# Kernel optimization log

Measured on AMD Instinct MI355X. Metric: run time of the kernel, lower is better.

## Reference

```python
import jax, jax.numpy as jnp
import numpy as np

# Config matching init_kwargs: N=4 networks, dims 128 -> 1024 -> 1024 -> 512
A, B, D = 8, 2048, 128     # agents, batch, input size
N = 4                       # number of independent SePS networks
H1, H2, H3 = 1024, 1024, 512


def setup_inputs() -> dict:
    key = jax.random.key(0)
    ks = jax.random.split(key, 6)
    inputs = jax.random.normal(ks[0], (A, B, D), dtype=jnp.float32)  # stacked per-agent obs
    seps_indices = jax.random.randint(ks[1], (B, A), 0, N)           # cluster id per (sample, agent)
    scale = lambda k, shape, fan: jax.random.normal(k, shape, dtype=jnp.float32) * (1.0 / np.sqrt(fan))
    W0 = scale(ks[2], (N, D, H1), D);   b0 = jnp.zeros((N, H1), jnp.float32)
    W1 = scale(ks[3], (N, H1, H2), H1); b1 = jnp.zeros((N, H2), jnp.float32)
    W2 = scale(ks[4], (N, H2, H3), H2); b2 = jnp.zeros((N, H3), jnp.float32)
    return {"inputs": inputs, "seps_indices": seps_indices,
            "W0": W0, "b0": b0, "W1": W1, "b1": b1, "W2": W2, "b2": b2}


def reference(inputs, seps_indices, W0, b0, W1, b1, W2, b2):
    # Run every network densely on the full stacked input, as the torch module does.
    # inputs: [A, B, D]; W*: [N, in, out]
    h = jax.nn.relu(jnp.einsum('abd,ndh->nabh', inputs, W0) + b0[:, None, None, :])
    h = jax.nn.relu(jnp.einsum('nabh,nhk->nabk', h, W1) + b1[:, None, None, :])
    out_all = jnp.einsum('nabk,nko->nabo', h, W2) + b2[:, None, None, :]  # [N, A, B, H3]
    # Gather along the network axis per (agent, sample): seps_indices is [B, A]
    idx = seps_indices.T                              # [A, B]
    a = jnp.arange(inputs.shape[0])[:, None]          # [A, 1]
    b = jnp.arange(inputs.shape[1])[None, :]          # [1, B]
    return out_all[idx, a, b, :]                      # [A, B, H3] (stacked per-agent outputs)
```

## Files before the change

### kernel.cpp

```cpp
#include <hip/hip_runtime.h>
#include <hip/hip_bf16.h>

#define AG 8
#define BT 2048
#define RT (AG*BT)
#define NNET 4
#define D0 128
#define H1 1024
#define H2 1024
#define H3 512

#define XBLK 40

typedef __attribute__((ext_vector_type(8))) short short8;
typedef __attribute__((ext_vector_type(4))) float f32x4;

__device__ __forceinline__ unsigned short f2bf(float f){
  unsigned int x = __float_as_uint(f);
  x += 0x7fff + ((x >> 16) & 1);
  return (unsigned short)(x >> 16);
}

template<int N> __device__ __forceinline__ void vmw(){
  if constexpr (N==8)      asm volatile("s_waitcnt vmcnt(8)" ::: "memory");
  else if constexpr (N==4) asm volatile("s_waitcnt vmcnt(4)" ::: "memory");
  else                     asm volatile("s_waitcnt vmcnt(0)" ::: "memory");
}

__device__ __forceinline__ void gload_lds16(const void* g, void* l){
  __builtin_amdgcn_global_load_lds(
      (const __attribute__((address_space(1))) unsigned int*)g,
      (__attribute__((address_space(3))) unsigned int*)l, 16, 0, 0);
}

__device__ __forceinline__ int bucket_off(const int* counts, int n){
  int s = 0;
  #pragma unroll
  for (int i = 0; i < NNET-1; i++) if (i < n) s += counts[i];
  return s;
}

__global__ void k_init(int* counts){
  if (threadIdx.x < NNET) counts[threadIdx.x] = 0;
}

__global__ __launch_bounds__(256) void k_compact(const int* __restrict__ seps,
                          int* __restrict__ counts, int* __restrict__ rowlist){
  __shared__ int lcount[NNET];
  __shared__ int lbase[NNET];
  int t = blockIdx.x * 256 + threadIdx.x;
  if (threadIdx.x < NNET) lcount[threadIdx.x] = 0;
  __syncthreads();
  int a = t >> 11, b = t & (BT-1);
  int n = seps[b*AG + a];
  int lrank = atomicAdd(&lcount[n], 1);
  __syncthreads();
  if (threadIdx.x < NNET)
    lbase[threadIdx.x] = atomicAdd(&counts[threadIdx.x], lcount[threadIdx.x]);
  __syncthreads();
  rowlist[n*RT + lbase[n] + lrank] = t;
}

template<int K, int NOUT>
__global__ __launch_bounds__(256) void k_transpose(const float* __restrict__ W,
                                                   unsigned short* __restrict__ WT){
  __shared__ float tile[32][33];
  int n = blockIdx.z;
  int k0 = blockIdx.x*32, o0 = blockIdx.y*32;
  const float* Wn = W + (size_t)n*K*NOUT;
  unsigned short* WTn = WT + (size_t)n*NOUT*K;
  int tx = threadIdx.x & 31, ty0 = threadIdx.x >> 5;
  #pragma unroll
  for (int r = 0; r < 32; r += 8)
    tile[ty0 + r][tx] = Wn[(size_t)(k0 + ty0 + r)*NOUT + o0 + tx];
  __syncthreads();
  #pragma unroll
  for (int r = 0; r < 32; r += 8)
    WTn[(size_t)(o0 + ty0 + r)*K + k0 + tx] = f2bf(tile[tx][ty0 + r]);
}

__global__ __launch_bounds__(256) void k_gather0(const float* __restrict__ X,
                          const int* __restrict__ counts,
                          const int* __restrict__ rowlist, unsigned short* __restrict__ X0h){
  int n = blockIdx.y;
  int cnt = counts[n];
  int i = blockIdx.x*16 + (threadIdx.x >> 4);
  if (i >= cnt) return;
  int off = bucket_off(counts, n);
  int orig = rowlist[n*RT + i];
  int c = (threadIdx.x & 15) * 8;
  const float* src = X + (size_t)orig*D0 + c;
  float4 v0 = *(const float4*)src, v1 = *(const float4*)(src+4);
  ushort4 u0, u1;
  u0.x=f2bf(v0.x); u0.y=f2bf(v0.y); u0.z=f2bf(v0.z); u0.w=f2bf(v0.w);
  u1.x=f2bf(v1.x); u1.y=f2bf(v1.y); u1.z=f2bf(v1.z); u1.w=f2bf(v1.w);
  unsigned short* dst = X0h + (size_t)(off + i)*D0 + c;
  *(ushort4*)dst = u0; *(ushort4*)(dst+4) = u1;
}

template<int K, int NOUT, int RELU, int SCATTER>
__global__ __launch_bounds__(256, 3) void k_mlp(
    const unsigned short* __restrict__ X,
    const unsigned short* __restrict__ WT,
    const float* __restrict__ Bias,
    const int* __restrict__ counts,
    const int* __restrict__ rowlist,
    unsigned short* __restrict__ Yh,
    float* __restrict__ Yf)
{
  constexpr int T = K / 32;
  const int n = blockIdx.z;
  const int cnt = counts[n];
  const int i0 = blockIdx.x * 128;
  if (i0 >= cnt) return;
  const int off = bucket_off(counts, n);
  const int bn = blockIdx.y * 128;

  __shared__ __align__(16) unsigned short As[3][128*32];
  __shared__ __align__(16) unsigned short Bs[3][128*32];
  __shared__ int rs[128];

  const int t = threadIdx.x, lane = t & 63, wave = t >> 6;
  const int wm = wave >> 1, wn = wave & 1;
  const int lr = lane & 15, g = lane >> 4;

  if (SCATTER && t < 128) rs[t] = rowlist[n*RT + min(i0 + t, cnt-1)];

  const unsigned short* pA[2]; const unsigned short* pB[2];
  unsigned int ldsoff[2];
  const unsigned short* WTn = WT + (size_t)n * NOUT * K;
  #pragma unroll
  for (int j = 0; j < 2; j++){
    int r  = (j*4 + wave)*16 + (lane >> 2);
    int ps = lane & 3;
    int ls = ps ^ ((r >> 1) & 3);
    int rA = min(i0 + r, cnt-1);
    pA[j] = X   + (size_t)(off + rA)*K + ls*8;
    pB[j] = WTn + (size_t)(bn  + r )*K + ls*8;
    ldsoff[j] = (unsigned)(j*4 + wave) * 512;
  }

  int aoff[4], boff[4];
  #pragma unroll
  for (int i = 0; i < 4; i++){
    int ra = wm*64 + i*16 + lr;
    aoff[i] = ra*32 + (g ^ ((ra>>1)&3))*8;
    int rb = wn*64 + i*16 + lr;
    boff[i] = rb*32 + (g ^ ((rb>>1)&3))*8;
  }

  __syncthreads();

  #pragma unroll
  for (int s = 0; s < 3; ++s){
    #pragma unroll
    for (int j = 0; j < 2; j++){
      gload_lds16(pA[j], &As[s][ldsoff[j]]);
      gload_lds16(pB[j], &Bs[s][ldsoff[j]]);
      pA[j] += 32; pB[j] += 32;
    }
  }

  f32x4 acc[4][4] = {};
  int b = 0;
  for (int ks = 0; ks < T; ++ks){
    if (ks < T-2)       vmw<8>();
    else if (ks == T-2) vmw<4>();
    else                vmw<0>();
    __builtin_amdgcn_s_barrier();

    short8 av[4], bv[4];
    #pragma unroll
    for (int i = 0; i < 4; i++) av[i] = *(const short8*)&As[b][aoff[i]];
    #pragma unroll
    for (int i = 0; i < 4; i++) bv[i] = *(const short8*)&Bs[b][boff[i]];

    #pragma unroll
    for (int mi = 0; mi < 4; mi++)
      #pragma unroll
      for (int ni = 0; ni < 4; ni++)
        acc[mi][ni] = __builtin_amdgcn_mfma_f32_16x16x32_bf16(bv[ni], av[mi], acc[mi][ni], 0, 0, 0);
    asm volatile("s_waitcnt lgkmcnt(0)" ::: "memory");
    __builtin_amdgcn_s_barrier();
    if (ks + 3 < T){
      #pragma unroll
      for (int j = 0; j < 2; j++){
        gload_lds16(pA[j], &As[b][ldsoff[j]]);
        gload_lds16(pB[j], &Bs[b][ldsoff[j]]);
        pA[j] += 32; pB[j] += 32;
      }
    }

    b = (b == 2) ? 0 : b + 1;
  }

  f32x4 bias4[4];
  #pragma unroll
  for (int ni = 0; ni < 4; ni++)
    bias4[ni] = *(const f32x4*)&Bias[n*NOUT + bn + wn*64 + ni*16 + (g<<2)];

  #pragma unroll
  for (int mi = 0; mi < 4; mi++){
    int rloc = wm*64 + mi*16 + lr;
    int grow = i0 + rloc;
    if (grow < cnt){
      #pragma unroll
      for (int ni = 0; ni < 4; ni++){
        float o[4];
        #pragma unroll
        for (int i = 0; i < 4; i++){
          float v = acc[mi][ni][i] + bias4[ni][i];
          if (RELU) v = fmaxf(v, 0.f);
          o[i] = v;
        }
        int cb = bn + wn*64 + ni*16 + (g<<2);
        if (SCATTER){
          *(float4*)&Yf[(size_t)rs[rloc]*NOUT + cb] = make_float4(o[0],o[1],o[2],o[3]);
        } else {
          ushort4 u;
          u.x=f2bf(o[0]); u.y=f2bf(o[1]); u.z=f2bf(o[2]); u.w=f2bf(o[3]);
          *(ushort4*)&Yh[(size_t)(off + grow)*NOUT + cb] = u;
        }
      }
    }
  }
}

extern "C" void kernel_launch(void* const* d_in, const int* in_sizes, int n_in,
                              void* d_out, int out_size, void* d_ws, size_t ws_size,
                              hipStream_t stream) {
  const float* inputs = (const float*)d_in[0];
  const int*   seps   = (const int*)  d_in[1];
  const float* W0     = (const float*)d_in[2];
  const float* b0     = (const float*)d_in[3];
  const float* W1     = (const float*)d_in[4];
  const float* b1     = (const float*)d_in[5];
  const float* W2     = (const float*)d_in[6];
  const float* b2     = (const float*)d_in[7];
  float* out = (float*)d_out;

  char* ws = (char*)d_ws;
  int* counts  = (int*)ws;
  int* rowlist = (int*)(ws + 4096);
  const size_t MB = 1u << 20;
  unsigned short* WT0 = (unsigned short*)(ws + 1*MB);
  unsigned short* WT1 = (unsigned short*)(ws + 2*MB);
  unsigned short* WT2 = (unsigned short*)(ws + 10*MB);
  unsigned short* h1  = (unsigned short*)(ws + 14*MB);
  unsigned short* h2  = (unsigned short*)(ws + 46*MB);
  unsigned short* X0h = (unsigned short*)(ws + 46*MB);

  k_init   <<<1, 64, 0, stream>>>(counts);
  k_compact<<<RT/256, 256, 0, stream>>>(seps, counts, rowlist);

  k_transpose<D0, H1><<<dim3(D0/32, H1/32, NNET), 256, 0, stream>>>(W0, WT0);
  k_transpose<H1, H2><<<dim3(H1/32, H2/32, NNET), 256, 0, stream>>>(W1, WT1);
  k_transpose<H2, H3><<<dim3(H2/32, H3/32, NNET), 256, 0, stream>>>(W2, WT2);
  k_gather0<<<dim3(RT/16, NNET), 256, 0, stream>>>(inputs, counts, rowlist, X0h);

  k_mlp<D0, H1, 1, 0><<<dim3(XBLK, H1/128, NNET), 256, 0, stream>>>(
      X0h, WT0, b0, counts, rowlist, h1, nullptr);
  k_mlp<H1, H2, 1, 0><<<dim3(XBLK, H2/128, NNET), 256, 0, stream>>>(
      h1, WT1, b1, counts, rowlist, h2, nullptr);
  k_mlp<H2, H3, 0, 1><<<dim3(XBLK, H3/128, NNET), 256, 0, stream>>>(
      h2, WT2, b2, counts, rowlist, nullptr, out);
}
```

Before: 135.5 us.

## Replace LDS-staged triple-buffered GEMM loads with direct global register loads

Removes the shared-memory tiles, the async global-to-LDS pipeline and the per-step barriers from the MLP GEMM kernel. Each wave now loads its A and B MFMA fragments straight from global memory into registers and relies on the cache for reuse across waves. This drops LDS traffic and synchronisation, but each tile is fetched from global memory or cache several times and there is no explicit prefetch to hide latency. The occupancy hint in the launch bounds is also removed.

```diff
diff --git a/kernel.cpp b/kernel.cpp
--- a/kernel.cpp
+++ b/kernel.cpp
@@ -19,18 +19,6 @@
   unsigned int x = __float_as_uint(f);
   x += 0x7fff + ((x >> 16) & 1);
   return (unsigned short)(x >> 16);
-}
-
-template<int N> __device__ __forceinline__ void vmw(){
-  if constexpr (N==8)      asm volatile("s_waitcnt vmcnt(8)" ::: "memory");
-  else if constexpr (N==4) asm volatile("s_waitcnt vmcnt(4)" ::: "memory");
-  else                     asm volatile("s_waitcnt vmcnt(0)" ::: "memory");
-}
-
-__device__ __forceinline__ void gload_lds16(const void* g, void* l){
-  __builtin_amdgcn_global_load_lds(
-      (const __attribute__((address_space(1))) unsigned int*)g,
-      (__attribute__((address_space(3))) unsigned int*)l, 16, 0, 0);
 }
 
 __device__ __forceinline__ int bucket_off(const int* counts, int n){
@@ -99,7 +87,7 @@
 }
 
 template<int K, int NOUT, int RELU, int SCATTER>
-__global__ __launch_bounds__(256, 3) void k_mlp(
+__global__ __launch_bounds__(256) void k_mlp(
     const unsigned short* __restrict__ X,
     const unsigned short* __restrict__ WT,
     const float* __restrict__ Bias,
@@ -116,82 +104,41 @@
   const int off = bucket_off(counts, n);
   const int bn = blockIdx.y * 128;
 
-  __shared__ __align__(16) unsigned short As[3][128*32];
-  __shared__ __align__(16) unsigned short Bs[3][128*32];
   __shared__ int rs[128];
 
   const int t = threadIdx.x, lane = t & 63, wave = t >> 6;
   const int wm = wave >> 1, wn = wave & 1;
   const int lr = lane & 15, g = lane >> 4;
 
-  if (SCATTER && t < 128) rs[t] = rowlist[n*RT + min(i0 + t, cnt-1)];
-
-  const unsigned short* pA[2]; const unsigned short* pB[2];
-  unsigned int ldsoff[2];
+  if (SCATTER){
+    if (t < 128) rs[t] = rowlist[n*RT + min(i0 + t, cnt-1)];
+    __syncthreads();
+  }
+
   const unsigned short* WTn = WT + (size_t)n * NOUT * K;
-  #pragma unroll
-  for (int j = 0; j < 2; j++){
-    int r  = (j*4 + wave)*16 + (lane >> 2);
-    int ps = lane & 3;
-    int ls = ps ^ ((r >> 1) & 3);
-    int rA = min(i0 + r, cnt-1);
-    pA[j] = X   + (size_t)(off + rA)*K + ls*8;
-    pB[j] = WTn + (size_t)(bn  + r )*K + ls*8;
-    ldsoff[j] = (unsigned)(j*4 + wave) * 512;
-  }
-
-  int aoff[4], boff[4];
+  const unsigned short* pa[4];
+  const unsigned short* pb[4];
   #pragma unroll
   for (int i = 0; i < 4; i++){
-    int ra = wm*64 + i*16 + lr;
-    aoff[i] = ra*32 + (g ^ ((ra>>1)&3))*8;
-    int rb = wn*64 + i*16 + lr;
-    boff[i] = rb*32 + (g ^ ((rb>>1)&3))*8;
-  }
-
-  __syncthreads();
-
-  #pragma unroll
-  for (int s = 0; s < 3; ++s){
-    #pragma unroll
-    for (int j = 0; j < 2; j++){
-      gload_lds16(pA[j], &As[s][ldsoff[j]]);
-      gload_lds16(pB[j], &Bs[s][ldsoff[j]]);
-      pA[j] += 32; pB[j] += 32;
-    }
+    int ra = min(i0 + wm*64 + i*16 + lr, cnt-1);
+    pa[i] = X + (size_t)(off + ra)*K + g*8;
+    int rb = bn + wn*64 + i*16 + lr;
+    pb[i] = WTn + (size_t)rb*K + g*8;
   }
 
   f32x4 acc[4][4] = {};
-  int b = 0;
+  #pragma unroll 2
   for (int ks = 0; ks < T; ++ks){
-    if (ks < T-2)       vmw<8>();
-    else if (ks == T-2) vmw<4>();
-    else                vmw<0>();
-    __builtin_amdgcn_s_barrier();
-
     short8 av[4], bv[4];
     #pragma unroll
-    for (int i = 0; i < 4; i++) av[i] = *(const short8*)&As[b][aoff[i]];
+    for (int i = 0; i < 4; i++){ av[i] = *(const short8*)pa[i]; pa[i] += 32; }
     #pragma unroll
-    for (int i = 0; i < 4; i++) bv[i] = *(const short8*)&Bs[b][boff[i]];
-
+    for (int i = 0; i < 4; i++){ bv[i] = *(const short8*)pb[i]; pb[i] += 32; }
     #pragma unroll
     for (int mi = 0; mi < 4; mi++)
       #pragma unroll
       for (int ni = 0; ni < 4; ni++)
         acc[mi][ni] = __builtin_amdgcn_mfma_f32_16x16x32_bf16(bv[ni], av[mi], acc[mi][ni], 0, 0, 0);
-    asm volatile("s_waitcnt lgkmcnt(0)" ::: "memory");
-    __builtin_amdgcn_s_barrier();
-    if (ks + 3 < T){
-      #pragma unroll
-      for (int j = 0; j < 2; j++){
-        gload_lds16(pA[j], &As[b][ldsoff[j]]);
-        gload_lds16(pB[j], &Bs[b][ldsoff[j]]);
-        pA[j] += 32; pB[j] += 32;
-      }
-    }
-
-    b = (b == 2) ? 0 : b + 1;
   }
 
   f32x4 bias4[4];
```

Result: slower. 301.2 us (+122.2%).

## Double-buffer LDS-to-register fragments to overlap reads with MFMA

Applied to the files above, without the earlier changes.

Restructures the grouped GEMM main loop so the LDS fragments for the next k-step are read into a second register set while MFMAs run on the current set. The loop is unrolled by two and drops one barrier per iteration, and the global-to-LDS prefetch is issued right after the single barrier. The aim is to hide LDS read latency behind matrix instructions. In exchange it uses more VGPRs for the second fragment set, and the unroll by two assumes T is even.

```diff
diff --git a/kernel.cpp b/kernel.cpp
--- a/kernel.cpp
+++ b/kernel.cpp
@@ -160,39 +160,56 @@
       pA[j] += 32; pB[j] += 32;
     }
   }
+  vmw<8>();
+  __builtin_amdgcn_s_barrier();
+  __builtin_amdgcn_sched_barrier(0);
+
+  short8 avA[4], bvA[4], avB[4], bvB[4];
+  #pragma unroll
+  for (int i = 0; i < 4; i++){
+    avA[i] = *(const short8*)&As[0][aoff[i]];
+    bvA[i] = *(const short8*)&Bs[0][boff[i]];
+  }
 
   f32x4 acc[4][4] = {};
-  int b = 0;
-  for (int ks = 0; ks < T; ++ks){
-    if (ks < T-2)       vmw<8>();
-    else if (ks == T-2) vmw<4>();
-    else                vmw<0>();
-    __builtin_amdgcn_s_barrier();
-
-    short8 av[4], bv[4];
-    #pragma unroll
-    for (int i = 0; i < 4; i++) av[i] = *(const short8*)&As[b][aoff[i]];
-    #pragma unroll
-    for (int i = 0; i < 4; i++) bv[i] = *(const short8*)&Bs[b][boff[i]];
-
-    #pragma unroll
-    for (int mi = 0; mi < 4; mi++)
-      #pragma unroll
-      for (int ni = 0; ni < 4; ni++)
-        acc[mi][ni] = __builtin_amdgcn_mfma_f32_16x16x32_bf16(bv[ni], av[mi], acc[mi][ni], 0, 0, 0);
-    asm volatile("s_waitcnt lgkmcnt(0)" ::: "memory");
-    __builtin_amdgcn_s_barrier();
-    if (ks + 3 < T){
-      #pragma unroll
-      for (int j = 0; j < 2; j++){
-        gload_lds16(pA[j], &As[b][ldsoff[j]]);
-        gload_lds16(pB[j], &Bs[b][ldsoff[j]]);
-        pA[j] += 32; pB[j] += 32;
-      }
-    }
-
-    b = (b == 2) ? 0 : b + 1;
-  }
+
+#define MLP_STEP(KS, CA, CB, NA, NB)                                          \
+  {                                                                           \
+    const int ks_ = (KS);                                                     \
+    if (ks_ < T-2) vmw<4>(); else vmw<0>();                                   \
+    asm volatile("s_waitcnt lgkmcnt(0)" ::: "memory");                        \
+    __builtin_amdgcn_s_barrier();                                             \
+    __builtin_amdgcn_sched_barrier(0);                                        \
+    if (ks_ + 3 < T){                                                         \
+      const int bd = ks_ % 3;                                                 \
+      _Pragma("unroll")                                                       \
+      for (int j = 0; j < 2; j++){                                            \
+        gload_lds16(pA[j], &As[bd][ldsoff[j]]);                               \
+        gload_lds16(pB[j], &Bs[bd][ldsoff[j]]);                               \
+        pA[j] += 32; pB[j] += 32;                                             \
+      }                                                                       \
+    }                                                                         \
+    if (ks_ + 1 < T){                                                         \
+      const int br = (ks_ + 1) % 3;                                           \
+      _Pragma("unroll")                                                       \
+      for (int i = 0; i < 4; i++){                                            \
+        NA[i] = *(const short8*)&As[br][aoff[i]];                             \
+        NB[i] = *(const short8*)&Bs[br][boff[i]];                             \
+      }                                                                       \
+    }                                                                         \
+    _Pragma("unroll")                                                         \
+    for (int mi = 0; mi < 4; mi++)                                            \
+      _Pragma("unroll")                                                       \
+      for (int ni = 0; ni < 4; ni++)                                          \
+        acc[mi][ni] = __builtin_amdgcn_mfma_f32_16x16x32_bf16(                \
+            CB[ni], CA[mi], acc[mi][ni], 0, 0, 0);                            \
+  }
+
+  for (int ks = 0; ks < T; ks += 2){
+    MLP_STEP(ks,   avA, bvA, avB, bvB);
+    MLP_STEP(ks+1, avB, bvB, avA, bvA);
+  }
+#undef MLP_STEP
 
   f32x4 bias4[4];
   #pragma unroll
```

New measurement: 134.7 us. Within noise of the previous version (-0.6%).
